# Kernel tuning notes

Measured on AMD Instinct MI355X. Metric: run time of the kernel, lower is better.

## Reference

```python
import jax, jax.numpy as jnp
import numpy as np

E = 2048        # embed_dim
HQ = 32         # num_query_heads
HKV = 8         # num_kv_heads
HD = E // HQ    # head_dim = 64
G = HQ // HKV   # queries per kv head = 4
B, T = 2, 2048


def setup_inputs() -> dict:
    key = jax.random.key(0)
    kx, kq, kkv, ko = jax.random.split(key, 4)
    s = 1.0 / np.sqrt(E)
    x = jax.random.normal(kx, (B, T, E), dtype=jnp.float32)
    Wq = jax.random.normal(kq, (E, E), dtype=jnp.float32) * s          # torch Linear weight (out,in)
    Wkv = jax.random.normal(kkv, (2 * HKV * HD, E), dtype=jnp.float32) * s
    Wo = jax.random.normal(ko, (E, E), dtype=jnp.float32) * s
    return {"x": x, "Wq": Wq, "Wkv": Wkv, "Wo": Wo}


def reference(x, Wq, Wkv, Wo):
    Bx, Tx, C = x.shape
    scale = 1.0 / np.sqrt(HD)
    # projections (torch Linear: y = x @ W.T)
    q = x @ Wq.T                                   # (B,T,E)
    kv = x @ Wkv.T                                 # (B,T,2*HKV*HD)
    k, v = jnp.split(kv, 2, axis=-1)               # each (B,T,HKV*HD)
    # grouped layout: q -> (B,HKV,G,T,HD); k,v -> (B,HKV,T,HD)
    q = q.reshape(Bx, Tx, HKV, G, HD).transpose(0, 2, 3, 1, 4)
    k = k.reshape(Bx, Tx, HKV, HD).transpose(0, 2, 1, 3)
    v = v.reshape(Bx, Tx, HKV, HD).transpose(0, 2, 1, 3)
    # scores: equivalent to repeat_interleave of K over query-head groups
    att = jnp.einsum('bhgtd,bhsd->bhgts', q, k) * scale   # (B,HKV,G,T,T)
    causal = jnp.triu(jnp.ones((Tx, Tx), dtype=bool), k=1)
    att = jnp.where(causal, -jnp.inf, att)
    att = jax.nn.softmax(att, axis=-1)
    out = jnp.einsum('bhgts,bhsd->bhgtd', att, v)          # (B,HKV,G,T,HD)
    out = out.transpose(0, 3, 1, 2, 4).reshape(Bx, Tx, C)  # (B,T,E)
    return out @ Wo.T
```

## Files before the change

### kernel.cpp

```cpp
#include <hip/hip_runtime.h>
#include <hip/hip_bf16.h>
#include <math.h>

#define GQA_B   2
#define GQA_T   2048
#define GQA_E   2048
#define GQA_HQ  32
#define GQA_HKV 8
#define GQA_HD  64
#define GQA_EKV 1024
#define GQA_M   (GQA_B * GQA_T)

typedef short  bf16x8 __attribute__((ext_vector_type(8)));
typedef float  f32x4  __attribute__((ext_vector_type(4)));

#define GLDS16(gsrc, ldst)                                                 \
  __builtin_amdgcn_global_load_lds(                                       \
      (const __attribute__((address_space(1))) void*)(gsrc),              \
      (__attribute__((address_space(3))) void*)(ldst), 16, 0, 0)

__device__ __forceinline__ ushort f2b(float f) {
  union { float f; unsigned u; } c; c.f = f;
  unsigned u = c.u;
  u += 0x7fffu + ((u >> 16) & 1u);
  return (ushort)(u >> 16);
}

__global__ __launch_bounds__(256) void cvt_f32_bf16(
    const float* __restrict__ src, ushort* __restrict__ dst, int n4) {
  int i = blockIdx.x * blockDim.x + threadIdx.x;
  const int stride = gridDim.x * blockDim.x;
  for (; i < n4; i += stride) {
    float4 v = *(const float4*)(src + (size_t)i * 4);
    ushort4 o;
    o.x = f2b(v.x); o.y = f2b(v.y); o.z = f2b(v.z); o.w = f2b(v.w);
    *(ushort4*)(dst + (size_t)i * 4) = o;
  }
}

__device__ __forceinline__ void store_out(ushort* p, float v) { *p = f2b(v); }
__device__ __forceinline__ void store_out(float* p, float v)  { *p = v; }

template <typename CT>
__global__ __launch_bounds__(256) void gemm_nt_bf16(
    const ushort* __restrict__ A, const ushort* __restrict__ B,
    CT* __restrict__ C, int M, int N, int K) {
  __shared__ __align__(16) ushort As[2 * 128 * 32];
  __shared__ __align__(16) ushort Bs[2 * 128 * 32];
  const int tid = threadIdx.x;
  const int l  = tid & 63;
  const int w  = tid >> 6;
  const int lm = l & 15;
  const int lg = l >> 4;
  const int wm = w & 1;
  const int wn = w >> 1;
  const int bm = blockIdx.y * 128;
  const int bn = blockIdx.x * 128;

  const int srow = w * 32 + (l >> 2);
  const int scol = (l & 3) * 8;
  const ushort* Ag = A + (size_t)(bm + srow) * K + scol;
  const ushort* Bg = B + (size_t)(bn + srow) * K + scol;
  char* ldsAw = (char*)As + w * 2048;
  char* ldsBw = (char*)Bs + w * 2048;

  f32x4 acc[4][4];
#pragma unroll
  for (int i = 0; i < 4; ++i)
#pragma unroll
    for (int j = 0; j < 4; ++j)
#pragma unroll
      for (int r = 0; r < 4; ++r) acc[i][j][r] = 0.f;

  const int nk = K >> 5;
  GLDS16(Ag,                  ldsAw);
  GLDS16(Ag + (size_t)16 * K, ldsAw + 1024);
  GLDS16(Bg,                  ldsBw);
  GLDS16(Bg + (size_t)16 * K, ldsBw + 1024);
  __syncthreads();

  int cur = 0;
  for (int ks = 0; ks < nk; ++ks) {
    if (ks + 1 < nk) {
      const size_t k0 = (size_t)(ks + 1) * 32;
      char* la = ldsAw + (cur ^ 1) * 8192;
      char* lb = ldsBw + (cur ^ 1) * 8192;
      GLDS16(Ag + k0,                  la);
      GLDS16(Ag + (size_t)16 * K + k0, la + 1024);
      GLDS16(Bg + k0,                  lb);
      GLDS16(Bg + (size_t)16 * K + k0, lb + 1024);
    }
    const ushort* Ac = As + cur * 4096;
    const ushort* Bc = Bs + cur * 4096;
    bf16x8 af[4], bfr[4];
#pragma unroll
    for (int mf = 0; mf < 4; ++mf)
      af[mf] = *(const bf16x8*)(Ac + (wm * 64 + mf * 16 + lm) * 32 + lg * 8);
#pragma unroll
    for (int nf = 0; nf < 4; ++nf)
      bfr[nf] = *(const bf16x8*)(Bc + (wn * 64 + nf * 16 + lm) * 32 + lg * 8);
#pragma unroll
    for (int mf = 0; mf < 4; ++mf)
#pragma unroll
      for (int nf = 0; nf < 4; ++nf)
        acc[mf][nf] = __builtin_amdgcn_mfma_f32_16x16x32_bf16(
            af[mf], bfr[nf], acc[mf][nf], 0, 0, 0);
    __syncthreads();
    cur ^= 1;
  }

#pragma unroll
  for (int mf = 0; mf < 4; ++mf)
#pragma unroll
    for (int nf = 0; nf < 4; ++nf)
#pragma unroll
      for (int r = 0; r < 4; ++r) {
        const int row = bm + wm * 64 + mf * 16 + lg * 4 + r;
        const int col = bn + wn * 64 + nf * 16 + lm;
        store_out(C + (size_t)row * N + col, acc[mf][nf][r]);
      }
}

__global__ __launch_bounds__(256) void gqa_attn_mfma(
    const ushort* __restrict__ Q, const ushort* __restrict__ KV,
    ushort* __restrict__ Oat) {
  const int T = GQA_T, EQ = GQA_E, EKV = GQA_EKV;
  const int qt  = (int)gridDim.x - 1 - (int)blockIdx.x;
  const int qt0 = qt * 64;
  const int hq  = blockIdx.y;
  const int b   = blockIdx.z;
  const int hkv = hq >> 2;

  __shared__ __align__(16) ushort Ks[2 * 64 * 64];
  __shared__ __align__(16) ushort Vt[2 * 64 * 64];
  __shared__ __align__(16) ushort Ps[4 * 16 * 64];

  const int tid = threadIdx.x;
  const int w  = tid >> 6;
  const int l  = tid & 63;
  const int lm = l & 15;
  const int lg = l >> 4;

  const size_t qrow = ((size_t)b * T + qt0 + 16 * w + lm) * EQ + hq * 64;
  const bf16x8 qa0 = *(const bf16x8*)(Q + qrow + lg * 8);
  const bf16x8 qa1 = *(const bf16x8*)(Q + qrow + 32 + lg * 8);

  f32x4 oacc[4];
#pragma unroll
  for (int nd = 0; nd < 4; ++nd)
#pragma unroll
    for (int r = 0; r < 4; ++r) oacc[nd][r] = 0.f;
  float m2 = -INFINITY, lsum = 0.f;
  const float SCL2 = 0.125f * 1.44269504088896f;

  const size_t kvbase = (size_t)b * T * EKV + hkv * 64;

  const int k_key  = w * 8 + (l >> 3);
  const int k_srcd = (((l & 7) ^ (l >> 3)) * 8);
  char* PsB = (char*)Ps + w * 2048;
  const int pswz = (lm & 7) << 4;
  const size_t vgbase = kvbase + 512 + (size_t)l * EKV + w * 8;

  const int nt = qt + 1;

  {
    const ushort* kg = KV + kvbase + (size_t)k_key * EKV + k_srcd;
    GLDS16(kg,                    (char*)Ks + w * 1024);
    GLDS16(kg + (size_t)32 * EKV, (char*)Ks + (4 + w) * 1024);
    int4 v0 = *(const int4*)(KV + vgbase);
    int4 v1 = *(const int4*)(KV + vgbase + 32);
    union { int4 v; ushort u[8]; } a, bq;
    a.v = v0; bq.v = v1;
#pragma unroll
    for (int j = 0; j < 8; ++j) {
      const int d0 = w * 8 + j;
      *(ushort*)((char*)Vt + d0 * 128 + ((2 * l) ^ ((d0 & 7) << 4))) = a.u[j];
      const int d1 = 32 + w * 8 + j;
      *(ushort*)((char*)Vt + d1 * 128 + ((2 * l) ^ ((d1 & 7) << 4))) = bq.u[j];
    }
  }
  __syncthreads();

  int cur = 0;
  for (int t = 0; t < nt; ++t) {
    const int s0 = t * 64;
    const bool pf = (t + 1 < nt);
    int4 nv0, nv1;
    if (pf) {
      const size_t s1 = (size_t)(t + 1) * 64;
      nv0 = *(const int4*)(KV + vgbase + s1 * EKV);
      nv1 = *(const int4*)(KV + vgbase + s1 * EKV + 32);
      const ushort* kg = KV + kvbase + (s1 + k_key) * EKV + k_srcd;
      char* kb = (char*)Ks + (cur ^ 1) * 8192;
      GLDS16(kg,                    kb + w * 1024);
      GLDS16(kg + (size_t)32 * EKV, kb + (4 + w) * 1024);
    }
    const char* KsB = (const char*)Ks + cur * 8192;
    const char* VtB = (const char*)Vt + cur * 8192;

    f32x4 sacc[4];
#pragma unroll
    for (int nf = 0; nf < 4; ++nf)
#pragma unroll
      for (int r = 0; r < 4; ++r) sacc[nf][r] = 0.f;
#pragma unroll
    for (int nf = 0; nf < 4; ++nf) {
      const int krow = nf * 16 + lm;
      const int swz = (krow & 7) << 4;
      bf16x8 kb0 = *(const bf16x8*)(KsB + krow * 128 + ((lg * 16) ^ swz));
      bf16x8 kb1 = *(const bf16x8*)(KsB + krow * 128 + ((64 + lg * 16) ^ swz));
      sacc[nf] = __builtin_amdgcn_mfma_f32_16x16x32_bf16(kb0, qa0, sacc[nf], 0, 0, 0);
      sacc[nf] = __builtin_amdgcn_mfma_f32_16x16x32_bf16(kb1, qa1, sacc[nf], 0, 0, 0);
    }

    const int qg = qt0 + 16 * w + lm;
    if (t == nt - 1) {
#pragma unroll
      for (int nf = 0; nf < 4; ++nf)
#pragma unroll
        for (int r = 0; r < 4; ++r) {
          const int sg = s0 + nf * 16 + lg * 4 + r;
          if (sg > qg) sacc[nf][r] = -INFINITY;
        }
    }

    float mt = -INFINITY;
#pragma unroll
    for (int nf = 0; nf < 4; ++nf)
#pragma unroll
      for (int r = 0; r < 4; ++r) mt = fmaxf(mt, sacc[nf][r]);
    mt = fmaxf(mt, __shfl_xor(mt, 16));
    mt = fmaxf(mt, __shfl_xor(mt, 32));
    const float mnew = fmaxf(m2, mt * SCL2);
    const float alpha = exp2f(m2 - mnew);
    m2 = mnew;
    float ssum = 0.f;
#pragma unroll
    for (int nf = 0; nf < 4; ++nf)
#pragma unroll
      for (int r = 0; r < 4; ++r) {
        const float p = exp2f(fmaf(sacc[nf][r], SCL2, -mnew));
        sacc[nf][r] = p;
        ssum += p;
      }
    ssum += __shfl_xor(ssum, 16);
    ssum += __shfl_xor(ssum, 32);
    lsum = lsum * alpha + ssum;

    float ar[4];
#pragma unroll
    for (int r = 0; r < 4; ++r) ar[r] = __shfl(alpha, lg * 4 + r);
#pragma unroll
    for (int nd = 0; nd < 4; ++nd)
#pragma unroll
      for (int r = 0; r < 4; ++r) oacc[nd][r] *= ar[r];

#pragma unroll
    for (int nf = 0; nf < 4; ++nf) {
      union { uint2 v; __hip_bfloat162 h[2]; } pk;
      pk.h[0] = __float22bfloat162_rn(make_float2(sacc[nf][0], sacc[nf][1]));
      pk.h[1] = __float22bfloat162_rn(make_float2(sacc[nf][2], sacc[nf][3]));
      *(uint2*)(PsB + lm * 128 + ((nf * 32 + lg * 8) ^ pswz)) = pk.v;
    }

    {
      bf16x8 pa0 = *(const bf16x8*)(PsB + lm * 128 + ((lg * 16) ^ pswz));
      bf16x8 pa1 = *(const bf16x8*)(PsB + lm * 128 + ((64 + lg * 16) ^ pswz));
#pragma unroll
      for (int nd = 0; nd < 4; ++nd) {
        const int vrow = nd * 16 + lm;
        const int vswz = (vrow & 7) << 4;
        bf16x8 vb0 = *(const bf16x8*)(VtB + vrow * 128 + ((lg * 16) ^ vswz));
        bf16x8 vb1 = *(const bf16x8*)(VtB + vrow * 128 + ((64 + lg * 16) ^ vswz));
        oacc[nd] = __builtin_amdgcn_mfma_f32_16x16x32_bf16(pa0, vb0, oacc[nd], 0, 0, 0);
        oacc[nd] = __builtin_amdgcn_mfma_f32_16x16x32_bf16(pa1, vb1, oacc[nd], 0, 0, 0);
      }
    }

    if (pf) {
      char* vb = (char*)Vt + (cur ^ 1) * 8192;
      union { int4 v; ushort u[8]; } a, bq;
      a.v = nv0; bq.v = nv1;
#pragma unroll
      for (int j = 0; j < 8; ++j) {
        const int d0 = w * 8 + j;
        *(ushort*)(vb + d0 * 128 + ((2 * l) ^ ((d0 & 7) << 4))) = a.u[j];
        const int d1 = 32 + w * 8 + j;
        *(ushort*)(vb + d1 * 128 + ((2 * l) ^ ((d1 & 7) << 4))) = bq.u[j];
      }
    }
    __syncthreads();
    cur ^= 1;
  }

  const float inv_own = 1.f / lsum;
  float ir[4];
#pragma unroll
  for (int r = 0; r < 4; ++r) ir[r] = __shfl(inv_own, lg * 4 + r);
  const size_t ob = ((size_t)b * T + qt0 + 16 * w + lg * 4) * EQ + hq * 64 + lm;
#pragma unroll
  for (int nd = 0; nd < 4; ++nd)
#pragma unroll
    for (int r = 0; r < 4; ++r)
      Oat[ob + (size_t)r * EQ + nd * 16] = f2b(oacc[nd][r] * ir[r]);
}

extern "C" void kernel_launch(void* const* d_in, const int* in_sizes, int n_in,
                              void* d_out, int out_size, void* d_ws, size_t ws_size,
                              hipStream_t stream) {
  const float* x   = (const float*)d_in[0];
  const float* Wq  = (const float*)d_in[1];
  const float* Wkv = (const float*)d_in[2];
  const float* Wo  = (const float*)d_in[3];
  float* out = (float*)d_out;

  ushort* xb   = (ushort*)d_ws;
  ushort* wqb  = xb   + (size_t)GQA_M * GQA_E;
  ushort* wkvb = wqb  + (size_t)GQA_E * GQA_E;
  ushort* wob  = wkvb + (size_t)GQA_EKV * GQA_E;
  ushort* qb   = wob  + (size_t)GQA_E * GQA_E;
  ushort* kvb  = qb   + (size_t)GQA_M * GQA_E;
  ushort* attb = kvb  + (size_t)GQA_M * GQA_EKV;

  cvt_f32_bf16<<<2048, 256, 0, stream>>>(x,   xb,   GQA_M * GQA_E / 4);
  cvt_f32_bf16<<<1024, 256, 0, stream>>>(Wq,  wqb,  GQA_E * GQA_E / 4);
  cvt_f32_bf16<<<512,  256, 0, stream>>>(Wkv, wkvb, GQA_EKV * GQA_E / 4);
  cvt_f32_bf16<<<1024, 256, 0, stream>>>(Wo,  wob,  GQA_E * GQA_E / 4);

  gemm_nt_bf16<ushort><<<dim3(GQA_E / 128, GQA_M / 128), 256, 0, stream>>>(
      xb, wqb, qb, GQA_M, GQA_E, GQA_E);
  gemm_nt_bf16<ushort><<<dim3(GQA_EKV / 128, GQA_M / 128), 256, 0, stream>>>(
      xb, wkvb, kvb, GQA_M, GQA_EKV, GQA_E);
  gqa_attn_mfma<<<dim3(GQA_T / 64, GQA_HQ, GQA_B), 256, 0, stream>>>(
      qb, kvb, attb);
  gemm_nt_bf16<float><<<dim3(GQA_E / 128, GQA_M / 128), 256, 0, stream>>>(
      attb, wob, out, GQA_M, GQA_E, GQA_E);
}
```

Baseline: 422.5 us.

## Double query tile per attention block and add lazy softmax rescaling

The attention kernel now handles 128 query rows per block, with two 16-row fragments per wave, so each K/V tile loaded into shared memory feeds twice as many MFMAs. It also skips the running-max rescale of the accumulators unless the new max exceeds the old by a threshold, and raises wave priority around the MFMA sections. This halves K/V traffic and block count per head, but doubles register use and shared P buffers, and the grid of 16x32x2 blocks is coarser, which may hurt load balance under the causal mask.

```diff
diff --git a/kernel.cpp b/kernel.cpp
--- a/kernel.cpp
+++ b/kernel.cpp
@@ -126,14 +126,14 @@
     ushort* __restrict__ Oat) {
   const int T = GQA_T, EQ = GQA_E, EKV = GQA_EKV;
   const int qt  = (int)gridDim.x - 1 - (int)blockIdx.x;
-  const int qt0 = qt * 64;
+  const int qt0 = qt * 128;
   const int hq  = blockIdx.y;
   const int b   = blockIdx.z;
   const int hkv = hq >> 2;
 
   __shared__ __align__(16) ushort Ks[2 * 64 * 64];
   __shared__ __align__(16) ushort Vt[2 * 64 * 64];
-  __shared__ __align__(16) ushort Ps[4 * 16 * 64];
+  __shared__ __align__(16) ushort Ps[4 * 32 * 64];
 
   const int tid = threadIdx.x;
   const int w  = tid >> 6;
@@ -141,27 +141,34 @@
   const int lm = l & 15;
   const int lg = l >> 4;
 
-  const size_t qrow = ((size_t)b * T + qt0 + 16 * w + lm) * EQ + hq * 64;
-  const bf16x8 qa0 = *(const bf16x8*)(Q + qrow + lg * 8);
-  const bf16x8 qa1 = *(const bf16x8*)(Q + qrow + 32 + lg * 8);
-
-  f32x4 oacc[4];
-#pragma unroll
-  for (int nd = 0; nd < 4; ++nd)
-#pragma unroll
-    for (int r = 0; r < 4; ++r) oacc[nd][r] = 0.f;
-  float m2 = -INFINITY, lsum = 0.f;
+  const size_t qr0 = ((size_t)b * T + qt0 + 32 * w + lm) * EQ + hq * 64;
+  bf16x8 qa[2][2];
+  qa[0][0] = *(const bf16x8*)(Q + qr0 + lg * 8);
+  qa[0][1] = *(const bf16x8*)(Q + qr0 + 32 + lg * 8);
+  qa[1][0] = *(const bf16x8*)(Q + qr0 + (size_t)16 * EQ + lg * 8);
+  qa[1][1] = *(const bf16x8*)(Q + qr0 + (size_t)16 * EQ + 32 + lg * 8);
+
+  f32x4 oacc[2][4];
+#pragma unroll
+  for (int fq = 0; fq < 2; ++fq)
+#pragma unroll
+    for (int nd = 0; nd < 4; ++nd)
+#pragma unroll
+      for (int r = 0; r < 4; ++r) oacc[fq][nd][r] = 0.f;
+  float m2[2]  = {-INFINITY, -INFINITY};
+  float lsum[2] = {0.f, 0.f};
   const float SCL2 = 0.125f * 1.44269504088896f;
+  const float THR2 = 11.5f;
 
   const size_t kvbase = (size_t)b * T * EKV + hkv * 64;
 
   const int k_key  = w * 8 + (l >> 3);
   const int k_srcd = (((l & 7) ^ (l >> 3)) * 8);
-  char* PsB = (char*)Ps + w * 2048;
+  char* PsB = (char*)Ps + w * 4096;
   const int pswz = (lm & 7) << 4;
   const size_t vgbase = kvbase + 512 + (size_t)l * EKV + w * 8;
 
-  const int nt = qt + 1;
+  const int nt = 2 * qt + 2;
 
   {
     const ushort* kg = KV + kvbase + (size_t)k_key * EKV + k_srcd;
@@ -198,83 +205,119 @@
     const char* KsB = (const char*)Ks + cur * 8192;
     const char* VtB = (const char*)Vt + cur * 8192;
 
-    f32x4 sacc[4];
-#pragma unroll
-    for (int nf = 0; nf < 4; ++nf)
-#pragma unroll
-      for (int r = 0; r < 4; ++r) sacc[nf][r] = 0.f;
+    f32x4 sacc[2][4];
+#pragma unroll
+    for (int fq = 0; fq < 2; ++fq)
+#pragma unroll
+      for (int nf = 0; nf < 4; ++nf)
+#pragma unroll
+        for (int r = 0; r < 4; ++r) sacc[fq][nf][r] = 0.f;
+    __builtin_amdgcn_s_setprio(1);
 #pragma unroll
     for (int nf = 0; nf < 4; ++nf) {
       const int krow = nf * 16 + lm;
       const int swz = (krow & 7) << 4;
       bf16x8 kb0 = *(const bf16x8*)(KsB + krow * 128 + ((lg * 16) ^ swz));
       bf16x8 kb1 = *(const bf16x8*)(KsB + krow * 128 + ((64 + lg * 16) ^ swz));
-      sacc[nf] = __builtin_amdgcn_mfma_f32_16x16x32_bf16(kb0, qa0, sacc[nf], 0, 0, 0);
-      sacc[nf] = __builtin_amdgcn_mfma_f32_16x16x32_bf16(kb1, qa1, sacc[nf], 0, 0, 0);
-    }
-
-    const int qg = qt0 + 16 * w + lm;
-    if (t == nt - 1) {
+#pragma unroll
+      for (int fq = 0; fq < 2; ++fq) {
+        sacc[fq][nf] = __builtin_amdgcn_mfma_f32_16x16x32_bf16(kb0, qa[fq][0], sacc[fq][nf], 0, 0, 0);
+        sacc[fq][nf] = __builtin_amdgcn_mfma_f32_16x16x32_bf16(kb1, qa[fq][1], sacc[fq][nf], 0, 0, 0);
+      }
+    }
+    __builtin_amdgcn_s_setprio(0);
+
+    const int qw0 = qt0 + 32 * w;
+    if (s0 + 63 > qw0) {
+#pragma unroll
+      for (int fq = 0; fq < 2; ++fq) {
+        const int qg = qw0 + fq * 16 + lm;
+#pragma unroll
+        for (int nf = 0; nf < 4; ++nf)
+#pragma unroll
+          for (int r = 0; r < 4; ++r) {
+            const int sg = s0 + nf * 16 + lg * 4 + r;
+            if (sg > qg) sacc[fq][nf][r] = -INFINITY;
+          }
+      }
+    }
+
+    float mt[2];
+#pragma unroll
+    for (int fq = 0; fq < 2; ++fq) {
+      float m = -INFINITY;
 #pragma unroll
       for (int nf = 0; nf < 4; ++nf)
 #pragma unroll
+        for (int r = 0; r < 4; ++r) m = fmaxf(m, sacc[fq][nf][r]);
+      m = fmaxf(m, __shfl_xor(m, 16));
+      m = fmaxf(m, __shfl_xor(m, 32));
+      mt[fq] = m * SCL2;
+    }
+    const bool small_ = (mt[0] <= m2[0] + THR2) && (mt[1] <= m2[1] + THR2);
+    if (!__all(small_)) {
+#pragma unroll
+      for (int fq = 0; fq < 2; ++fq) {
+        const float mn = fmaxf(m2[fq], mt[fq]);
+        const float al = exp2f(m2[fq] - mn);
+        m2[fq] = mn;
+        lsum[fq] *= al;
+        float ar[4];
+#pragma unroll
+        for (int r = 0; r < 4; ++r) ar[r] = __shfl(al, lg * 4 + r);
+#pragma unroll
+        for (int nd = 0; nd < 4; ++nd)
+#pragma unroll
+          for (int r = 0; r < 4; ++r) oacc[fq][nd][r] *= ar[r];
+      }
+    }
+#pragma unroll
+    for (int fq = 0; fq < 2; ++fq) {
+      float ssum = 0.f;
+#pragma unroll
+      for (int nf = 0; nf < 4; ++nf)
+#pragma unroll
         for (int r = 0; r < 4; ++r) {
-          const int sg = s0 + nf * 16 + lg * 4 + r;
-          if (sg > qg) sacc[nf][r] = -INFINITY;
+          const float p = exp2f(fmaf(sacc[fq][nf][r], SCL2, -m2[fq]));
+          sacc[fq][nf][r] = p;
+          ssum += p;
         }
-    }
-
-    float mt = -INFINITY;
-#pragma unroll
-    for (int nf = 0; nf < 4; ++nf)
-#pragma unroll
-      for (int r = 0; r < 4; ++r) mt = fmaxf(mt, sacc[nf][r]);
-    mt = fmaxf(mt, __shfl_xor(mt, 16));
-    mt = fmaxf(mt, __shfl_xor(mt, 32));
-    const float mnew = fmaxf(m2, mt * SCL2);
-    const float alpha = exp2f(m2 - mnew);
-    m2 = mnew;
-    float ssum = 0.f;
-#pragma unroll
-    for (int nf = 0; nf < 4; ++nf)
-#pragma unroll
-      for (int r = 0; r < 4; ++r) {
-        const float p = exp2f(fmaf(sacc[nf][r], SCL2, -mnew));
-        sacc[nf][r] = p;
-        ssum += p;
-      }
-    ssum += __shfl_xor(ssum, 16);
-    ssum += __shfl_xor(ssum, 32);
-    lsum = lsum * alpha + ssum;
-
-    float ar[4];
-#pragma unroll
-    for (int r = 0; r < 4; ++r) ar[r] = __shfl(alpha, lg * 4 + r);
-#pragma unroll
-    for (int nd = 0; nd < 4; ++nd)
-#pragma unroll
-      for (int r = 0; r < 4; ++r) oacc[nd][r] *= ar[r];
-
-#pragma unroll
-    for (int nf = 0; nf < 4; ++nf) {
-      union { uint2 v; __hip_bfloat162 h[2]; } pk;
-      pk.h[0] = __float22bfloat162_rn(make_float2(sacc[nf][0], sacc[nf][1]));
-      pk.h[1] = __float22bfloat162_rn(make_float2(sacc[nf][2], sacc[nf][3]));
-      *(uint2*)(PsB + lm * 128 + ((nf * 32 + lg * 8) ^ pswz)) = pk.v;
-    }
+      ssum += __shfl_xor(ssum, 16);
+      ssum += __shfl_xor(ssum, 32);
+      lsum[fq] += ssum;
+    }
+
+#pragma unroll
+    for (int fq = 0; fq < 2; ++fq)
+#pragma unroll
+      for (int nf = 0; nf < 4; ++nf) {
+        union { uint2 v; __hip_bfloat162 h[2]; } pk;
+        pk.h[0] = __float22bfloat162_rn(make_float2(sacc[fq][nf][0], sacc[fq][nf][1]));
+        pk.h[1] = __float22bfloat162_rn(make_float2(sacc[fq][nf][2], sacc[fq][nf][3]));
+        *(uint2*)(PsB + fq * 2048 + lm * 128 + ((nf * 32 + lg * 8) ^ pswz)) = pk.v;
+      }
 
     {
-      bf16x8 pa0 = *(const bf16x8*)(PsB + lm * 128 + ((lg * 16) ^ pswz));
-      bf16x8 pa1 = *(const bf16x8*)(PsB + lm * 128 + ((64 + lg * 16) ^ pswz));
+      bf16x8 pa[2][2];
+#pragma unroll
+      for (int fq = 0; fq < 2; ++fq) {
+        pa[fq][0] = *(const bf16x8*)(PsB + fq * 2048 + lm * 128 + ((lg * 16) ^ pswz));
+        pa[fq][1] = *(const bf16x8*)(PsB + fq * 2048 + lm * 128 + ((64 + lg * 16) ^ pswz));
+      }
+      __builtin_amdgcn_s_setprio(1);
 #pragma unroll
       for (int nd = 0; nd < 4; ++nd) {
         const int vrow = nd * 16 + lm;
         const int vswz = (vrow & 7) << 4;
         bf16x8 vb0 = *(const bf16x8*)(VtB + vrow * 128 + ((lg * 16) ^ vswz));
         bf16x8 vb1 = *(const bf16x8*)(VtB + vrow * 128 + ((64 + lg * 16) ^ vswz));
-        oacc[nd] = __builtin_amdgcn_mfma_f32_16x16x32_bf16(pa0, vb0, oacc[nd], 0, 0, 0);
-        oacc[nd] = __builtin_amdgcn_mfma_f32_16x16x32_bf16(pa1, vb1, oacc[nd], 0, 0, 0);
-      }
+#pragma unroll
+        for (int fq = 0; fq < 2; ++fq) {
+          oacc[fq][nd] = __builtin_amdgcn_mfma_f32_16x16x32_bf16(pa[fq][0], vb0, oacc[fq][nd], 0, 0, 0);
+          oacc[fq][nd] = __builtin_amdgcn_mfma_f32_16x16x32_bf16(pa[fq][1], vb1, oacc[fq][nd], 0, 0, 0);
+        }
+      }
+      __builtin_amdgcn_s_setprio(0);
     }
 
     if (pf) {
@@ -293,16 +336,19 @@
     cur ^= 1;
   }
 
-  const float inv_own = 1.f / lsum;
-  float ir[4];
-#pragma unroll
-  for (int r = 0; r < 4; ++r) ir[r] = __shfl(inv_own, lg * 4 + r);
-  const size_t ob = ((size_t)b * T + qt0 + 16 * w + lg * 4) * EQ + hq * 64 + lm;
-#pragma unroll
-  for (int nd = 0; nd < 4; ++nd)
-#pragma unroll
-    for (int r = 0; r < 4; ++r)
-      Oat[ob + (size_t)r * EQ + nd * 16] = f2b(oacc[nd][r] * ir[r]);
+#pragma unroll
+  for (int fq = 0; fq < 2; ++fq) {
+    const float inv_own = 1.f / lsum[fq];
+    float ir[4];
+#pragma unroll
+    for (int r = 0; r < 4; ++r) ir[r] = __shfl(inv_own, lg * 4 + r);
+    const size_t ob = ((size_t)b * T + qt0 + 32 * w + fq * 16 + lg * 4) * EQ + hq * 64 + lm;
+#pragma unroll
+    for (int nd = 0; nd < 4; ++nd)
+#pragma unroll
+      for (int r = 0; r < 4; ++r)
+        Oat[ob + (size_t)r * EQ + nd * 16] = f2b(oacc[fq][nd][r] * ir[r]);
+  }
 }
 
 extern "C" void kernel_launch(void* const* d_in, const int* in_sizes, int n_in,
@@ -331,7 +377,7 @@
       xb, wqb, qb, GQA_M, GQA_E, GQA_E);
   gemm_nt_bf16<ushort><<<dim3(GQA_EKV / 128, GQA_M / 128), 256, 0, stream>>>(
       xb, wkvb, kvb, GQA_M, GQA_EKV, GQA_E);
-  gqa_attn_mfma<<<dim3(GQA_T / 64, GQA_HQ, GQA_B), 256, 0, stream>>>(
+  gqa_attn_mfma<<<dim3(GQA_T / 128, GQA_HQ, GQA_B), 256, 0, stream>>>(
       qb, kvb, attb);
   gemm_nt_bf16<float><<<dim3(GQA_E / 128, GQA_M / 128), 256, 0, stream>>>(
       attb, wob, out, GQA_M, GQA_E, GQA_E);
```

New measurement: 431.5 us. 2.1% more time.
